# Performance work log

Measured on AMD Instinct MI355X. Metric: run time of the kernel, lower is better.

## Reference

```python
import jax, jax.numpy as jnp
import numpy as np

HEADS = 16
HIDDEN = 1024
D_HEAD = HIDDEN // HEADS
SCALE = float(D_HEAD) ** 0.5


def setup_inputs() -> dict:
    key = jax.random.key(0)
    ks = jax.random.split(key, 11)
    B, L = 2, 2048
    x = jax.random.normal(ks[0], (B, L, HIDDEN), dtype=jnp.float32)
    # 0/1 padding mask, broadcast over heads and query positions
    mask = jax.random.randint(ks[1], (B, 1, 1, L), 0, 2).astype(jnp.float32)
    s = 1.0 / np.sqrt(HIDDEN)
    Wq = jax.random.normal(ks[2], (HIDDEN, HIDDEN), dtype=jnp.float32) * s
    bq = jax.random.normal(ks[3], (HIDDEN,), dtype=jnp.float32) * s
    Wk = jax.random.normal(ks[4], (HIDDEN, HIDDEN), dtype=jnp.float32) * s
    bk = jax.random.normal(ks[5], (HIDDEN,), dtype=jnp.float32) * s
    Wv = jax.random.normal(ks[6], (HIDDEN, HIDDEN), dtype=jnp.float32) * s
    bv = jax.random.normal(ks[7], (HIDDEN,), dtype=jnp.float32) * s
    Wo = jax.random.normal(ks[8], (HIDDEN, HIDDEN), dtype=jnp.float32) * s
    bo = jax.random.normal(ks[9], (HIDDEN,), dtype=jnp.float32) * s
    return {"x": x, "mask": mask, "Wq": Wq, "bq": bq, "Wk": Wk, "bk": bk,
            "Wv": Wv, "bv": bv, "Wo": Wo, "bo": bo}


def reference(x, mask, Wq, bq, Wk, bk, Wv, bv, Wo, bo):
    B, L, _ = x.shape
    # projections (Linear: x @ W + b), split heads -> [B, H, L, Dh]
    def proj(W, b):
        return (jnp.dot(x, W) + b).reshape(B, L, HEADS, D_HEAD).transpose(0, 2, 1, 3)
    q = proj(Wq, bq)
    k = proj(Wk, bk)
    v = proj(Wv, bv)
    # scaled dot-product with additive mask: scores [B, H, Lq, Lk]
    scores = jnp.einsum('bhqd,bhkd->bhqk', q, k) / SCALE + mask * (-10000.0)
    attn = jax.nn.softmax(scores, axis=-1)  # dropout p=0.0 -> identity
    out = jnp.einsum('bhqk,bhkd->bhqd', attn, v)
    out = out.transpose(0, 2, 1, 3).reshape(B, L, HIDDEN)
    return jnp.dot(out, Wo) + bo
```

## Files before the change

### kernel.cpp

```cpp
#include <hip/hip_runtime.h>
#include <math.h>

typedef unsigned short u16;
typedef short v8s __attribute__((ext_vector_type(8)));
typedef float v4f __attribute__((ext_vector_type(4)));
typedef float v16f __attribute__((ext_vector_type(16)));

#define HIDDEN 1024
#define L_SEQ 2048
#define NH 16
#define DH 64
#define NKMAX 1280

#define QSCALE 0.18033688011112042f

__device__ __forceinline__ u16 f2bf(float f) {
  union { float f; unsigned int i; } c; c.f = f;
  unsigned int x = c.i;
  unsigned int r = (x + 0x7fffu + ((x >> 16) & 1u)) >> 16;
  return (u16)r;
}

#if defined(__has_builtin)
#if __has_builtin(__builtin_amdgcn_cvt_pk_bf16_f32)
#define HAS_PKBF 1
#endif
#if __has_builtin(__builtin_amdgcn_exp2f)
#define EXP2(x) __builtin_amdgcn_exp2f(x)
#endif
#if __has_builtin(__builtin_amdgcn_rcpf)
#define RCP(x) __builtin_amdgcn_rcpf(x)
#endif
#endif
#ifndef EXP2
#define EXP2(x) exp2f(x)
#endif
#ifndef RCP
#define RCP(x) (1.0f / (x))
#endif

__device__ __forceinline__ unsigned pkbf(float a, float b) {
#ifdef HAS_PKBF
  typedef __bf16 v2bf __attribute__((ext_vector_type(2)));
  union { v2bf v; unsigned u; } c;
  c.v = __builtin_amdgcn_cvt_pk_bf16_f32(a, b);
  return c.u;
#else
  return (unsigned)f2bf(a) | ((unsigned)f2bf(b) << 16);
#endif
}

__device__ __forceinline__ void gload16(const void* g, void* l) {
  void* gg = const_cast<void*>(g);
  __builtin_amdgcn_global_load_lds(
      (__attribute__((address_space(1))) void*)gg,
      (__attribute__((address_space(3))) void*)l, 16, 0, 0);
}

__device__ __forceinline__ v16f vzero16() {
  v16f z;
#pragma unroll
  for (int i = 0; i < 16; ++i) z[i] = 0.f;
  return z;
}

__global__ __launch_bounds__(256) void prep(
    const float* __restrict__ x, u16* __restrict__ xb,
    const float* __restrict__ Wq, const float* __restrict__ Wk,
    const float* __restrict__ Wv, const float* __restrict__ Wo,
    u16* __restrict__ WtQ, u16* __restrict__ WtK,
    u16* __restrict__ WtV, u16* __restrict__ WtO,
    const float* __restrict__ maskg, u16* __restrict__ keep,
    unsigned* __restrict__ nkslot) {
  const int bid = blockIdx.x;
  const int t = threadIdx.x;

  if (bid < 2048) {
    const int i = (bid * 256 + t) * 8;
    const float4 a = *(const float4*)(x + i);
    const float4 b = *(const float4*)(x + i + 4);
    unsigned o[4] = {pkbf(a.x, a.y), pkbf(a.z, a.w), pkbf(b.x, b.y), pkbf(b.z, b.w)};
    *(uint4*)(xb + i) = *(const uint4*)o;
    return;
  }

  if (bid < 6144) {
    const int m = bid - 2048;
    const int z = m >> 10;
    const int rem = m & 1023;
    const int bx = rem & 31, by = rem >> 5;
    const float* src; u16* dst;
    if (z == 0) { src = Wq; dst = WtQ; }
    else if (z == 1) { src = Wk; dst = WtK; }
    else if (z == 2) { src = Wv; dst = WtV; }
    else { src = Wo; dst = WtO; }

    __shared__ u16 tile[32][33];
    const int tx = t & 31, ty = t >> 5;
    const int xcol = bx * 32 + tx;
    const int y0 = by * 32;
#pragma unroll
    for (int i = ty; i < 32; i += 8)
      tile[i][tx] = f2bf(src[(size_t)(y0 + i) * HIDDEN + xcol]);
    __syncthreads();
    const int xo = y0 + tx;
#pragma unroll
    for (int i = ty; i < 32; i += 8)
      dst[(size_t)(bx * 32 + i) * HIDDEN + xo] = tile[tx][i];
    return;
  }

  if (t < 64) {
    const int b = bid - 6144;
    const int lane = t;
    const float* mp = maskg + b * L_SEQ;
    int cnt = 0;
#pragma unroll 1
    for (int j = 0; j < 32; ++j) cnt += (mp[lane * 32 + j] == 0.0f) ? 1 : 0;
    int inc = cnt;
#pragma unroll
    for (int off = 1; off < 64; off <<= 1) {
      const int v = __shfl_up(inc, off, 64);
      if (lane >= off) inc += v;
    }
    int base = inc - cnt;
    u16* kp = keep + b * L_SEQ;
#pragma unroll 1
    for (int j = 0; j < 32; ++j) {
      const int k = lane * 32 + j;
      if (mp[k] == 0.0f) kp[base++] = (u16)k;
    }
    const int total = __shfl(inc, 63, 64);
    for (int i = total + lane; i < NKMAX; i += 64) kp[i] = 0;
    if (lane == 0) nkslot[b] = (unsigned)total;
  }
}

__global__ __launch_bounds__(256) void gemm128(
    const u16* __restrict__ A,
    const u16* __restrict__ B0, const u16* __restrict__ B1, const u16* __restrict__ B2,
    const float* __restrict__ bias0, const float* __restrict__ bias1, const float* __restrict__ bias2,
    u16* __restrict__ C0, u16* __restrict__ C1, u16* __restrict__ C2,
    float* __restrict__ Cf, const u16* __restrict__ keep,
    const unsigned* __restrict__ nkslot,
    int qkv_mode) {
  __shared__ __align__(16) u16 As[128 * 64];
  __shared__ __align__(16) u16 Bs[128 * 64];

  const int wgid = blockIdx.x;
  const int xcd = wgid & 7;
  const int j = wgid >> 3;
  const int bx = j & 7;
  const int rem = j >> 3;
  const int by = xcd * 4 + (rem & 3);
  const int bz = rem >> 2;

  const u16* Bt; const float* bias; u16* C;
  if (bz == 0) { Bt = B0; bias = bias0; C = C0; }
  else if (bz == 1) { Bt = B1; bias = bias1; C = C1; }
  else { Bt = B2; bias = bias2; C = C2; }
  const int mode = qkv_mode ? (bz == 0 ? 1 : (bz == 1 ? 2 : 3)) : 0;
  const float oscale = (mode == 1) ? QSCALE : 1.0f;

  const int t = threadIdx.x;
  const int lane = t & 63;
  const int wave = t >> 6;
  const int quad = lane >> 4;
  const int l16 = lane & 15;
  const int wm = wave >> 1;
  const int wn = wave & 1;

  const int n0 = bx * 128;

  const int r0 = t >> 3;
  const int og = ((t & 7) ^ (r0 & 7)) * 8;

  int m0 = by * 128;
  int kvb = 0;
  const u16* Ag[4];
  if (mode == 2 || mode == 3) {
    if (by >= 20) return;
    kvb = by / 10;
    m0 = (by % 10) * 128;
    const unsigned nk = nkslot[kvb];
    if ((unsigned)m0 >= ((nk + 63u) & ~63u)) return;
#pragma unroll
    for (int c = 0; c < 4; ++c) {
      const int rr = keep[kvb * L_SEQ + m0 + r0 + 32 * c];
      Ag[c] = A + ((size_t)(kvb * L_SEQ + rr)) * HIDDEN + og;
    }
  } else {
#pragma unroll
    for (int c = 0; c < 4; ++c)
      Ag[c] = A + (size_t)(m0 + r0 + 32 * c) * HIDDEN + og;
  }
  const u16* Bg0 = Bt + (size_t)(n0 + r0) * HIDDEN + og;

  u16* const Ald = As + t * 8;
  u16* const Bld = Bs + t * 8;

  v4f acc[4][4];
#pragma unroll
  for (int mi = 0; mi < 4; ++mi)
#pragma unroll
    for (int ni = 0; ni < 4; ++ni)
      acc[mi][ni] = (v4f){0.f, 0.f, 0.f, 0.f};

  for (int k0 = 0; k0 < HIDDEN; k0 += 64) {
    __syncthreads();
#pragma unroll
    for (int c = 0; c < 4; ++c) {
      gload16(Ag[c] + k0, Ald + 2048 * c);
      gload16(Bg0 + (size_t)(32 * c) * HIDDEN + k0, Bld + 2048 * c);
    }
    __syncthreads();

#pragma unroll
    for (int kk = 0; kk < 2; ++kk) {
      v8s a[4], b[4];
#pragma unroll
      for (int mi = 0; mi < 4; ++mi) {
        const int row = wm * 64 + mi * 16 + l16;
        a[mi] = *(const v8s*)&As[row * 64 + (((kk * 4 + quad) ^ (row & 7)) * 8)];
      }
#pragma unroll
      for (int ni = 0; ni < 4; ++ni) {
        const int row = wn * 64 + ni * 16 + l16;
        b[ni] = *(const v8s*)&Bs[row * 64 + (((kk * 4 + quad) ^ (row & 7)) * 8)];
      }
#pragma unroll
      for (int mi = 0; mi < 4; ++mi)
#pragma unroll
        for (int ni = 0; ni < 4; ++ni)
          acc[mi][ni] = __builtin_amdgcn_mfma_f32_16x16x32_bf16(a[mi], b[ni], acc[mi][ni], 0, 0, 0);
    }
  }

#pragma unroll
  for (int ni = 0; ni < 4; ++ni) {
    const int col = n0 + wn * 64 + ni * 16 + l16;
    const float bv = bias[col];
#pragma unroll
    for (int mi = 0; mi < 4; ++mi) {
      const int row0 = m0 + wm * 64 + mi * 16 + quad * 4;
      const float v0 = (acc[mi][ni][0] + bv) * oscale;
      const float v1 = (acc[mi][ni][1] + bv) * oscale;
      const float v2 = (acc[mi][ni][2] + bv) * oscale;
      const float v3 = (acc[mi][ni][3] + bv) * oscale;
      if (mode == 0) {
        Cf[(size_t)(row0 + 0) * HIDDEN + col] = v0;
        Cf[(size_t)(row0 + 1) * HIDDEN + col] = v1;
        Cf[(size_t)(row0 + 2) * HIDDEN + col] = v2;
        Cf[(size_t)(row0 + 3) * HIDDEN + col] = v3;
      } else if (mode == 1) {
        const int hh = col >> 6, d = col & 63;
        const float vv[4] = {v0, v1, v2, v3};
#pragma unroll
        for (int i = 0; i < 4; ++i) {
          const int rr = row0 + i;
          const int bb = rr >> 11, l = rr & 2047;
          C[((size_t)(bb * NH + hh) * L_SEQ + l) * DH + d] = f2bf(vv[i]);
        }
      } else if (mode == 2) {
        const int hh = col >> 6, d = col & 63;
        const float vv[4] = {v0, v1, v2, v3};
#pragma unroll
        for (int i = 0; i < 4; ++i)
          C[((size_t)(kvb * NH + hh) * L_SEQ + row0 + i) * DH + d] = f2bf(vv[i]);
      } else {
        const int hh = col >> 6, d = col & 63;
        unsigned pk[2] = {pkbf(v0, v1), pkbf(v2, v3)};
        *(uint2*)&C[((size_t)((kvb * NH + hh) * DH + d)) * L_SEQ + row0] = *(const uint2*)pk;
      }
    }
  }
}

#define XCH(D0_, D2_, A_, B_)                                        \
  {                                                                  \
    unsigned a_ = (A_), b_ = (B_);                                   \
    asm("v_permlane32_swap_b32 %0, %1" : "+v"(a_), "+v"(b_));        \
    D0_ = a_;                                      \
    D2_ = b_;                                      \
  }

#define MKPF(dst, P0, P1, P2, P3, P4, P5, P6, P7)                    \
  {                                                                  \
    const unsigned A_ = pkbf(P0, P1), C_ = pkbf(P2, P3);             \
    const unsigned B_ = pkbf(P4, P5), D_ = pkbf(P6, P7);             \
    union { unsigned u[4]; v8s v; } f_;                              \
    XCH(f_.u[0], f_.u[2], A_, B_);                                   \
    XCH(f_.u[1], f_.u[3], C_, D_);                                   \
    dst = f_.v;                                                      \
  }

__global__ __launch_bounds__(512) void attn512(
    const u16* __restrict__ Qg, const u16* __restrict__ Kcg, const u16* __restrict__ VTg,
    const unsigned* __restrict__ nkslot, u16* __restrict__ Og) {
  __shared__ __align__(16) u16 lds[32768];

  const int t = threadIdx.x;
  const int lane = t & 63;
  const int w = t >> 6;
  const int l31 = lane & 31;
  const int hi = lane >> 5;
  const int e7 = l31 & 7;

  const int bid = blockIdx.x;
  const int bh = bid & 31;
  const int q0 = (bid >> 5) * 256;
  const int b = bh >> 4;
  const int h = bh & 15;

  const size_t base = (size_t)bh * L_SEQ * DH;
  const u16* Qp = Qg + base;
  const u16* Kp = Kcg + base;
  const u16* VTp = VTg + base;

  const int nkb = (int)nkslot[b];
  const int ntiles = (nkb + 127) >> 7;

  const int r8 = lane >> 3, sl8 = lane & 7;
  const int koff = (w * 8 + r8) * DH + (sl8 ^ r8) * 8;
  const int r4 = lane >> 4, sl16 = lane & 15;
  const int vrow = w * 4 + r4;
  const int voff = vrow * L_SEQ + ((((sl16 & 7) ^ (vrow & 7)) | (sl16 & 8)) * 8);
  u16* const kd = &lds[(w * 8) * 64];
  u16* const vd = &lds[16384 + (w * 4) * 128];

  gload16(Kp + koff, kd);
  gload16(Kp + 64 * DH + koff, kd + 64 * 64);
  gload16(VTp + voff, vd);
  gload16(VTp + 32 * L_SEQ + voff, vd + 32 * 128);

  const int qrow = q0 + w * 32 + l31;
  v8s qf[4];
#pragma unroll
  for (int dc = 0; dc < 4; ++dc)
    qf[dc] = *(const v8s*)&Qp[(size_t)qrow * DH + dc * 16 + hi * 8];

  v16f oacc0 = vzero16(), oacc1 = vzero16();
  float lsum = 0.f;

  for (int n = 0; n < ntiles; ++n) {
    __syncthreads();
    const int ksb = (n & 1) * 8192;
    const int vtb = 16384 + (n & 1) * 8192;
    if (n + 1 < ntiles) {
      const size_t k1 = (size_t)(n + 1) * 128;
      const int s2 = ((n + 1) & 1) * 8192;
      gload16(Kp + k1 * DH + koff, kd + s2);
      gload16(Kp + (k1 + 64) * DH + koff, kd + s2 + 64 * 64);
      gload16(VTp + k1 + voff, vd + s2);
      gload16(VTp + k1 + 32 * L_SEQ + voff, vd + s2 + 32 * 128);
    }

    const int kb0 = n * 128;
#pragma unroll
    for (int hh = 0; hh < 2; ++hh) {
      const int h2 = hh ^ (w >> 2);
      v16f s0 = vzero16(), s1 = vzero16();
      __builtin_amdgcn_s_setprio(1);
#pragma unroll
      for (int dc = 0; dc < 4; ++dc) {
        const int po = ((dc * 2 + hi) ^ e7) * 8;
        const v8s kf0 = *(const v8s*)&lds[ksb + (h2 * 64 + l31) * 64 + po];
        const v8s kf1 = *(const v8s*)&lds[ksb + (h2 * 64 + 32 + l31) * 64 + po];
        s0 = __builtin_amdgcn_mfma_f32_32x32x16_bf16(kf0, qf[dc], s0, 0, 0, 0);
        s1 = __builtin_amdgcn_mfma_f32_32x32x16_bf16(kf1, qf[dc], s1, 0, 0, 0);
      }
      __builtin_amdgcn_s_setprio(0);

      const int kh0 = kb0 + h2 * 64;
      float p[32];
#pragma unroll
      for (int r = 0; r < 16; ++r) {
        p[r]      = EXP2(s0[r]);
        p[16 + r] = EXP2(s1[r]);
      }
      if (kh0 + 64 > nkb) {
#pragma unroll
        for (int r = 0; r < 16; ++r) {
          const int kk = kh0 + (r & 3) + 8 * (r >> 2) + 4 * hi;
          if (kk >= nkb) p[r] = 0.f;
          if (kk + 32 >= nkb) p[16 + r] = 0.f;
        }
      }
      {
        float a0 = 0.f, a1 = 0.f, a2 = 0.f, a3 = 0.f;
#pragma unroll
        for (int r = 0; r < 8; ++r) {
          a0 += p[r]; a1 += p[8 + r]; a2 += p[16 + r]; a3 += p[24 + r];
        }
        lsum += (a0 + a1) + (a2 + a3);
      }

      v8s pf0, pf1, pf2, pf3;
      MKPF(pf0, p[0],  p[1],  p[2],  p[3],  p[4],  p[5],  p[6],  p[7]);
      MKPF(pf1, p[8],  p[9],  p[10], p[11], p[12], p[13], p[14], p[15]);
      MKPF(pf2, p[16], p[17], p[18], p[19], p[20], p[21], p[22], p[23]);
      MKPF(pf3, p[24], p[25], p[26], p[27], p[28], p[29], p[30], p[31]);

      __builtin_amdgcn_s_setprio(1);
#pragma unroll
      for (int kc = 0; kc < 4; ++kc) {
        const v8s pb = (kc == 0) ? pf0 : (kc == 1) ? pf1 : (kc == 2) ? pf2 : pf3;
        const int oc = h2 * 8 + kc * 2 + hi;
        const int po = (((oc & 7) ^ e7) | (oc & 8)) * 8;
        const v8s vf0 = *(const v8s*)&lds[vtb + l31 * 128 + po];
        const v8s vf1 = *(const v8s*)&lds[vtb + (32 + l31) * 128 + po];
        oacc0 = __builtin_amdgcn_mfma_f32_32x32x16_bf16(vf0, pb, oacc0, 0, 0, 0);
        oacc1 = __builtin_amdgcn_mfma_f32_32x32x16_bf16(vf1, pb, oacc1, 0, 0, 0);
      }
      __builtin_amdgcn_s_setprio(0);
    }
  }

  const float ltot = lsum + __shfl(lsum, lane ^ 32, 64);
  const float linv = RCP(ltot);

  const size_t ob = ((size_t)(b * L_SEQ + qrow)) * HIDDEN + h * DH;
#pragma unroll
  for (int r = 0; r < 16; r += 2) {
    const int d0 = (r & 3) + 8 * (r >> 2) + 4 * hi;
    const unsigned w0 = pkbf(oacc0[r] * linv, oacc0[r + 1] * linv);
    const unsigned w1 = pkbf(oacc1[r] * linv, oacc1[r + 1] * linv);
    *(unsigned*)&Og[ob + d0] = w0;
    *(unsigned*)&Og[ob + 32 + d0] = w1;
  }
}

extern "C" void kernel_launch(void* const* d_in, const int* in_sizes, int n_in,
                              void* d_out, int out_size, void* d_ws, size_t ws_size,
                              hipStream_t stream) {
  const float* x    = (const float*)d_in[0];
  const float* mask = (const float*)d_in[1];
  const float* Wq   = (const float*)d_in[2];
  const float* bq   = (const float*)d_in[3];
  const float* Wk   = (const float*)d_in[4];
  const float* bk   = (const float*)d_in[5];
  const float* Wv   = (const float*)d_in[6];
  const float* bv   = (const float*)d_in[7];
  const float* Wo   = (const float*)d_in[8];
  const float* bo   = (const float*)d_in[9];
  float* out = (float*)d_out;
  u16* ws = (u16*)d_ws;

  const unsigned M1 = 1u << 20;
  u16* WtQ = ws;
  u16* WtK = ws + M1;
  u16* WtV = ws + 2 * M1;
  u16* WtO = ws + 3 * M1;
  u16* xb  = ws + 4 * M1;
  u16* Qb  = ws + 8 * M1;
  u16* Kc  = ws + 12 * M1;
  u16* VTc = ws + 16 * M1;
  u16* Ob  = ws + 20 * M1;
  u16* keep = ws + 16 * M1 - 8192;
  unsigned* nkslot = (unsigned*)(ws + 16 * M1 - 8192 - 8);

  prep<<<6146, 256, 0, stream>>>(x, xb, Wq, Wk, Wv, Wo, WtQ, WtK, WtV, WtO,
                                 mask, keep, nkslot);
  gemm128<<<dim3(768), 256, 0, stream>>>(xb, WtQ, WtK, WtV, bq, bk, bv,
                                         Qb, Kc, VTc, nullptr, keep, nkslot, 1);
  attn512<<<dim3(256), 512, 0, stream>>>(Qb, Kc, VTc, nkslot, Ob);
  gemm128<<<dim3(256), 256, 0, stream>>>(Ob, WtO, WtO, WtO, bo, bo, bo,
                                         nullptr, nullptr, nullptr, out, nullptr, nullptr, 0);
}
```

Baseline: 187.5 us.

## Double-buffer GEMM LDS tiles with async prefetch two stages ahead

Converts the single-buffered LDS tile loop in the projection GEMM into a two-slot ring. Global-to-LDS loads for stage n+2 are issued while stage n is computed, and explicit vmcnt/lgkmcnt waits plus raw barriers replace the pair of __syncthreads. MFMA sections run at raised wave priority via s_setprio. This doubles LDS use per block to 64KB, which can lower occupancy, and the hand-written waitcnt counts must match the number of outstanding loads per stage.

```diff
diff --git a/kernel.cpp b/kernel.cpp
--- a/kernel.cpp
+++ b/kernel.cpp
@@ -144,8 +144,8 @@
     float* __restrict__ Cf, const u16* __restrict__ keep,
     const unsigned* __restrict__ nkslot,
     int qkv_mode) {
-  __shared__ __align__(16) u16 As[128 * 64];
-  __shared__ __align__(16) u16 Bs[128 * 64];
+  __shared__ __align__(16) u16 As[2 * 128 * 64];
+  __shared__ __align__(16) u16 Bs[2 * 128 * 64];
 
   const int wgid = blockIdx.x;
   const int xcd = wgid & 7;
@@ -196,9 +196,6 @@
   }
   const u16* Bg0 = Bt + (size_t)(n0 + r0) * HIDDEN + og;
 
-  u16* const Ald = As + t * 8;
-  u16* const Bld = Bs + t * 8;
-
   v4f acc[4][4];
 #pragma unroll
   for (int mi = 0; mi < 4; ++mi)
@@ -206,27 +203,40 @@
     for (int ni = 0; ni < 4; ++ni)
       acc[mi][ni] = (v4f){0.f, 0.f, 0.f, 0.f};
 
-  for (int k0 = 0; k0 < HIDDEN; k0 += 64) {
-    __syncthreads();
+  auto STAGE = [&](int n) {
+    const int bo = (n & 1) * 8192;
+    const int k0 = n * 64;
+    u16* const Ald = As + bo + t * 8;
+    u16* const Bld = Bs + bo + t * 8;
 #pragma unroll
     for (int c = 0; c < 4; ++c) {
       gload16(Ag[c] + k0, Ald + 2048 * c);
       gload16(Bg0 + (size_t)(32 * c) * HIDDEN + k0, Bld + 2048 * c);
     }
-    __syncthreads();
-
+  };
+
+  STAGE(0);
+  STAGE(1);
+
+  for (int n = 0; n < 16; ++n) {
+    if (n < 15) asm volatile("s_waitcnt vmcnt(8)" ::: "memory");
+    else        asm volatile("s_waitcnt vmcnt(0)" ::: "memory");
+    __builtin_amdgcn_s_barrier();
+    const int cur = (n & 1) * 8192;
+
+    __builtin_amdgcn_s_setprio(1);
 #pragma unroll
     for (int kk = 0; kk < 2; ++kk) {
       v8s a[4], b[4];
 #pragma unroll
       for (int mi = 0; mi < 4; ++mi) {
         const int row = wm * 64 + mi * 16 + l16;
-        a[mi] = *(const v8s*)&As[row * 64 + (((kk * 4 + quad) ^ (row & 7)) * 8)];
+        a[mi] = *(const v8s*)&As[cur + row * 64 + (((kk * 4 + quad) ^ (row & 7)) * 8)];
       }
 #pragma unroll
       for (int ni = 0; ni < 4; ++ni) {
         const int row = wn * 64 + ni * 16 + l16;
-        b[ni] = *(const v8s*)&Bs[row * 64 + (((kk * 4 + quad) ^ (row & 7)) * 8)];
+        b[ni] = *(const v8s*)&Bs[cur + row * 64 + (((kk * 4 + quad) ^ (row & 7)) * 8)];
       }
 #pragma unroll
       for (int mi = 0; mi < 4; ++mi)
@@ -234,6 +244,11 @@
         for (int ni = 0; ni < 4; ++ni)
           acc[mi][ni] = __builtin_amdgcn_mfma_f32_16x16x32_bf16(a[mi], b[ni], acc[mi][ni], 0, 0, 0);
     }
+    __builtin_amdgcn_s_setprio(0);
+
+    asm volatile("s_waitcnt lgkmcnt(0)" ::: "memory");
+    __builtin_amdgcn_s_barrier();
+    if (n + 2 < 16) STAGE(n + 2);
   }
 
 #pragma unroll
```

After: 191.9 us. 1.02x slower.
